# Kernel tuning notes

Measured on AMD Instinct MI355X. Metric: run time of the kernel, lower is better.

The kernel has to match this reference:

```python
import jax, jax.numpy as jnp
import numpy as np

B, S, H = 4, 2048, 1024
NH = 16
HD = H // NH  # 64
EPS = 1e-12


def setup_inputs() -> dict:
    key = jax.random.key(0)
    ks = jax.random.split(key, 10)
    sc = 1.0 / np.sqrt(H)
    return {
        "hidden_states": jax.random.normal(ks[0], (B, S, H), jnp.float32),
        "attention_mask": jnp.ones((B, S), jnp.float32),
        "Wq": jax.random.normal(ks[1], (H, H), jnp.float32) * sc,
        "bq": jnp.zeros((H,), jnp.float32),
        "Wk": jax.random.normal(ks[2], (H, H), jnp.float32) * sc,
        "bk": jnp.zeros((H,), jnp.float32),
        "Wv": jax.random.normal(ks[3], (H, H), jnp.float32) * sc,
        "bv": jnp.zeros((H,), jnp.float32),
        "Wd": jax.random.normal(ks[4], (H, H), jnp.float32) * sc,
        "bd": jnp.zeros((H,), jnp.float32),
        "ln_g": jnp.ones((H,), jnp.float32),
        "ln_b": jnp.zeros((H,), jnp.float32),
    }


def reference(hidden_states, attention_mask, Wq, bq, Wk, bk, Wv, bv, Wd, bd, ln_g, ln_b):
    def heads(x):  # [B,S,H] -> [B,NH,S,HD]
        return x.reshape(B, S, NH, HD).transpose(0, 2, 1, 3)

    q = heads(hidden_states @ Wq.T + bq)
    k = heads(hidden_states @ Wk.T + bk)
    v = heads(hidden_states @ Wv.T + bv)

    scores = jnp.einsum('bhqd,bhkd->bhqk', q, k) / np.sqrt(HD).astype(np.float32)
    # 2D mask -> [B,1,1,S]; (1-m)*-10000 additive bias
    bias = (1.0 - attention_mask)[:, None, None, :] * -10000.0
    probs = jax.nn.softmax(scores + bias, axis=-1)  # dropout p=0 -> identity

    ctx = jnp.einsum('bhqk,bhkd->bhqd', probs, v)
    ctx = ctx.transpose(0, 2, 1, 3).reshape(B, S, H)

    out = ctx @ Wd.T + bd
    x = out + hidden_states
    mu = jnp.mean(x, axis=-1, keepdims=True)
    var = jnp.mean(jnp.square(x - mu), axis=-1, keepdims=True)
    return (x - mu) * jax.lax.rsqrt(var + EPS) * ln_g + ln_b
```

## Files before the change

### kernel.cpp

```cpp
#include <hip/hip_runtime.h>
#include <stdint.h>

#define B_ 4
#define S_ 2048
#define H_ 1024
#define NH_ 16
#define HD_ 64

typedef __bf16 bf16x8 __attribute__((ext_vector_type(8)));
typedef unsigned short u16x8 __attribute__((ext_vector_type(8)));
typedef float f32x4 __attribute__((ext_vector_type(4)));
typedef float f32x16 __attribute__((ext_vector_type(16)));

__device__ __forceinline__ unsigned short f2bf(float x) {
  union { float f; unsigned u; } c; c.f = x;
  unsigned r = (c.u + 0x7FFFu + ((c.u >> 16) & 1u)) >> 16;
  return (unsigned short)r;
}

__device__ __forceinline__ void gload16(const unsigned short* g, unsigned short* lds) {
  __builtin_amdgcn_global_load_lds((const __attribute__((address_space(1))) void*)g,
                                   (__attribute__((address_space(3))) void*)lds, 16, 0, 0);
}

__global__ __launch_bounds__(256) void cvt_kernel(const float* __restrict__ src,
                                                  unsigned short* __restrict__ dst, int n) {
  int i = (blockIdx.x * blockDim.x + threadIdx.x) * 4;
  if (i < n) {
    float4 v = *reinterpret_cast<const float4*>(src + i);
    ushort4 o;
    o.x = f2bf(v.x); o.y = f2bf(v.y); o.z = f2bf(v.z); o.w = f2bf(v.w);
    *reinterpret_cast<ushort4*>(dst + i) = o;
  }
}

template <bool BF16OUT>
__global__ __launch_bounds__(256) void gemm_bt(const unsigned short* __restrict__ A,
                                               const unsigned short* __restrict__ Bm,
                                               const float* __restrict__ bias,
                                               void* __restrict__ Cout,
                                               int M, int N, int K) {
  __shared__ unsigned short As[128 * 32];
  __shared__ unsigned short Bs[128 * 32];
  const int t = threadIdx.x;
  const int lane = t & 63;
  const int wv = t >> 6;
  const int wm = wv >> 1, wn = wv & 1;
  const int m0 = blockIdx.x * 128, n0 = blockIdx.y * 128;
  const int l15 = lane & 15, g8 = (lane >> 4) * 8;

  f32x4 acc[4][4];
#pragma unroll
  for (int i = 0; i < 4; ++i)
#pragma unroll
    for (int j = 0; j < 4; ++j) { f32x4 z = {0.f, 0.f, 0.f, 0.f}; acc[i][j] = z; }

  const int rowA = t >> 2;
  const int colA = (t & 3) * 8;
  const unsigned short* gA0 = A + (long)(m0 + rowA) * K + colA;
  const unsigned short* gA1 = A + (long)(m0 + 64 + rowA) * K + colA;
  const unsigned short* gB0 = Bm + (long)(n0 + rowA) * K + colA;
  const unsigned short* gB1 = Bm + (long)(n0 + 64 + rowA) * K + colA;
  unsigned short* ldsA0 = &As[wv * 512];
  unsigned short* ldsA1 = &As[2048 + wv * 512];
  unsigned short* ldsB0 = &Bs[wv * 512];
  unsigned short* ldsB1 = &Bs[2048 + wv * 512];

  for (int k0 = 0; k0 < K; k0 += 32) {
    __syncthreads();
    gload16(gA0 + k0, ldsA0);
    gload16(gA1 + k0, ldsA1);
    gload16(gB0 + k0, ldsB0);
    gload16(gB1 + k0, ldsB1);
    __syncthreads();

    bf16x8 af[4], bfr[4];
#pragma unroll
    for (int i = 0; i < 4; ++i)
      af[i] = *reinterpret_cast<const bf16x8*>(&As[(wm * 64 + i * 16 + l15) * 32 + g8]);
#pragma unroll
    for (int j = 0; j < 4; ++j)
      bfr[j] = *reinterpret_cast<const bf16x8*>(&Bs[(wn * 64 + j * 16 + l15) * 32 + g8]);
#pragma unroll
    for (int i = 0; i < 4; ++i)
#pragma unroll
      for (int j = 0; j < 4; ++j)
        acc[i][j] = __builtin_amdgcn_mfma_f32_16x16x32_bf16(af[i], bfr[j], acc[i][j], 0, 0, 0);
  }

  const int r0 = (lane >> 4) * 4;
#pragma unroll
  for (int i = 0; i < 4; ++i)
#pragma unroll
    for (int j = 0; j < 4; ++j) {
      int col = n0 + wn * 64 + j * 16 + l15;
      float bv = bias[col];
#pragma unroll
      for (int r = 0; r < 4; ++r) {
        int row = m0 + wm * 64 + i * 16 + r0 + r;
        float v = acc[i][j][r] + bv;
        if (BF16OUT)
          ((unsigned short*)Cout)[(long)row * N + col] = f2bf(v);
        else
          ((float*)Cout)[(long)row * N + col] = v;
      }
    }
}

__global__ __launch_bounds__(256) void attn_kernel(const unsigned short* __restrict__ Q,
                                                   const unsigned short* __restrict__ Kg,
                                                   const unsigned short* __restrict__ Vg,
                                                   const float* __restrict__ mask,
                                                   unsigned short* __restrict__ ctx) {
  __shared__ __align__(16) unsigned short Kt[64 * 72];
  __shared__ __align__(16) unsigned short VtT[64 * 72];
  __shared__ __align__(16) float biasL[64];
  __shared__ __align__(16) float alBuf[4][32];
  __shared__ int mflag;

  const int t = threadIdx.x, lane = t & 63;
  const int wv = t >> 6;
  const int h = blockIdx.y, b = blockIdx.z;
  const int q0w = blockIdx.x * 128 + wv * 32;
  const int l31 = lane & 31, h2 = lane >> 5;
  const long headoff = (long)h * HD_;
  const float L2E = 1.44269504088896f;
  const float SC = 0.125f * L2E;

  bf16x8 qf[4];
  {
    const unsigned short* Qrow = Q + ((long)(b * S_ + q0w + l31)) * H_ + headoff;
#pragma unroll
    for (int c = 0; c < 4; ++c) {
      bf16x8 raw = *reinterpret_cast<const bf16x8*>(Qrow + 16 * c + 8 * h2);
#pragma unroll
      for (int j = 0; j < 8; ++j) qf[c][j] = (__bf16)((float)raw[j] * SC);
    }
  }

  f32x16 o[2];
#pragma unroll
  for (int dt = 0; dt < 2; ++dt)
#pragma unroll
    for (int r = 0; r < 16; ++r) o[dt][r] = 0.f;
  float mrow = -1.0e30f, lsum = 0.f;

  const unsigned short* KtA = &Kt[l31 * 72 + 8 * h2];
  const int rowd0 = l31, rowd1 = 32 + l31;
  const int grp0 = (rowd0 >> 3) & 7, grp1 = (rowd1 >> 3) & 7;

  for (int kv0 = 0; kv0 < S_; kv0 += 64) {
    __syncthreads();
#pragma unroll
    for (int it = 0; it < 2; ++it) {
      int job = t + it * 256;
      int kv = job >> 3, cg = (job & 7) * 8;
      u16x8 kvv = *reinterpret_cast<const u16x8*>(
          Kg + ((long)(b * S_ + kv0 + kv)) * H_ + headoff + cg);
      *reinterpret_cast<u16x8*>(&Kt[kv * 72 + cg]) = kvv;
    }
    {
      int p2 = t >> 3, dc = t & 7;
      int kv = p2 * 2;
      const unsigned short* vp0 = Vg + ((long)(b * S_ + kv0 + kv)) * H_ + headoff + dc * 8;
      u16x8 v0 = *reinterpret_cast<const u16x8*>(vp0);
      u16x8 v1 = *reinterpret_cast<const u16x8*>(vp0 + H_);
      int pos = (kv & 7) | (((kv >> 3) ^ dc) << 3);
#pragma unroll
      for (int j = 0; j < 8; ++j) {
        ushort2 pr; pr.x = v0[j]; pr.y = v1[j];
        *reinterpret_cast<ushort2*>(&VtT[(dc * 8 + j) * 72 + pos]) = pr;
      }
    }
    if (t < 64) {
      float mv = mask[b * S_ + kv0 + t];
      bool nz = (mv != 1.0f);
      biasL[t] = (1.f - mv) * (-10000.f * L2E);
      unsigned long long bal = __ballot(nz);
      if (t == 0) mflag = (bal != 0ull);
    }
    __syncthreads();

#pragma unroll
    for (int kvt = 0; kvt < 2; ++kvt) {
      f32x16 sv;
#pragma unroll
      for (int r = 0; r < 16; ++r) sv[r] = 0.f;
#pragma unroll
      for (int c = 0; c < 4; ++c) {
        bf16x8 af = *reinterpret_cast<const bf16x8*>(KtA + (kvt * 32) * 72 + 16 * c);
        sv = __builtin_amdgcn_mfma_f32_32x32x16_bf16(af, qf[c], sv, 0, 0, 0);
      }
      if (mflag) {
#pragma unroll
        for (int m = 0; m < 4; ++m) {
          f32x4 bb = *reinterpret_cast<const f32x4*>(&biasL[kvt * 32 + 8 * m + 4 * h2]);
#pragma unroll
          for (int i = 0; i < 4; ++i) sv[4 * m + i] += bb[i];
        }
      }
      float tm = sv[0];
#pragma unroll
      for (int r = 1; r < 16; ++r) tm = fmaxf(tm, sv[r]);
      tm = fmaxf(tm, __shfl_xor(tm, 32));
      if (!__all(tm <= mrow + 8.0f)) {
        float mn = fmaxf(mrow, tm);
        float al = exp2f(mrow - mn);
        mrow = mn;
        lsum *= al;
        if (lane < 32) alBuf[wv][lane] = al;
        __builtin_amdgcn_wave_barrier();
#pragma unroll
        for (int m = 0; m < 4; ++m) {
          f32x4 av = *reinterpret_cast<const f32x4*>(&alBuf[wv][8 * m + 4 * h2]);
#pragma unroll
          for (int i = 0; i < 4; ++i) {
            o[0][4 * m + i] *= av[i];
            o[1][4 * m + i] *= av[i];
          }
        }
      }
      float ts = 0.f;
#pragma unroll
      for (int r = 0; r < 16; ++r) {
        float p = exp2f(sv[r] - mrow);
        sv[r] = p;
        ts += p;
      }
      ts += __shfl_xor(ts, 32);
      lsum += ts;

#pragma unroll
      for (int c2 = 0; c2 < 2; ++c2) {
        int kc = 2 * kvt + c2;
        unsigned p0, p1, p2, p3;
        {
          union { __bf16 e[2]; unsigned w; } u;
          u.e[0] = (__bf16)sv[8 * c2 + 0]; u.e[1] = (__bf16)sv[8 * c2 + 1]; p0 = u.w;
          u.e[0] = (__bf16)sv[8 * c2 + 2]; u.e[1] = (__bf16)sv[8 * c2 + 3]; p1 = u.w;
          u.e[0] = (__bf16)sv[8 * c2 + 4]; u.e[1] = (__bf16)sv[8 * c2 + 5]; p2 = u.w;
          u.e[0] = (__bf16)sv[8 * c2 + 6]; u.e[1] = (__bf16)sv[8 * c2 + 7]; p3 = u.w;
        }
        asm("v_permlane32_swap_b32 %0, %1" : "+v"(p0), "+v"(p2));
        asm("v_permlane32_swap_b32 %0, %1" : "+v"(p1), "+v"(p3));
        union { unsigned w[4]; bf16x8 v; } fa;
        fa.w[0] = p0; fa.w[1] = p1; fa.w[2] = p2; fa.w[3] = p3;

        bf16x8 vb0 = *reinterpret_cast<const bf16x8*>(
            &VtT[rowd0 * 72 + 8 * ((2 * kc + h2) ^ grp0)]);
        bf16x8 vb1 = *reinterpret_cast<const bf16x8*>(
            &VtT[rowd1 * 72 + 8 * ((2 * kc + h2) ^ grp1)]);
        o[0] = __builtin_amdgcn_mfma_f32_32x32x16_bf16(fa.v, vb0, o[0], 0, 0, 0);
        o[1] = __builtin_amdgcn_mfma_f32_32x32x16_bf16(fa.v, vb1, o[1], 0, 0, 0);
      }
    }
  }

  if (lane < 32) alBuf[wv][lane] = 1.0f / lsum;
  __builtin_amdgcn_wave_barrier();
  unsigned short* ctxbase = ctx + ((long)(b * S_ + q0w + 4 * h2)) * H_ + headoff + l31;
#pragma unroll
  for (int m = 0; m < 4; ++m) {
    f32x4 iv = *reinterpret_cast<const f32x4*>(&alBuf[wv][8 * m + 4 * h2]);
#pragma unroll
    for (int i = 0; i < 4; ++i) {
#pragma unroll
      for (int dt = 0; dt < 2; ++dt)
        ctxbase[(long)(8 * m + i) * H_ + dt * 32] = f2bf(o[dt][4 * m + i] * iv[i]);
    }
  }
}

__global__ __launch_bounds__(256) void ln_kernel(const float* __restrict__ proj,
                                                 const float* __restrict__ hs,
                                                 const float* __restrict__ gam,
                                                 const float* __restrict__ bet,
                                                 float* __restrict__ out) {
  const int row = blockIdx.x;
  const int t = threadIdx.x;
  const long base = (long)row * H_ + t * 4;
  float4 a = *reinterpret_cast<const float4*>(proj + base);
  float4 hv = *reinterpret_cast<const float4*>(hs + base);
  float x0 = a.x + hv.x, x1 = a.y + hv.y, x2 = a.z + hv.z, x3 = a.w + hv.w;
  float s1 = x0 + x1 + x2 + x3;
  float s2 = x0 * x0 + x1 * x1 + x2 * x2 + x3 * x3;
#pragma unroll
  for (int off = 1; off < 64; off <<= 1) {
    s1 += __shfl_xor(s1, off);
    s2 += __shfl_xor(s2, off);
  }
  __shared__ float a1[4], a2[4];
  if ((t & 63) == 0) { a1[t >> 6] = s1; a2[t >> 6] = s2; }
  __syncthreads();
  float ts1 = a1[0] + a1[1] + a1[2] + a1[3];
  float ts2 = a2[0] + a2[1] + a2[2] + a2[3];
  float mu = ts1 * (1.0f / H_);
  float var = ts2 * (1.0f / H_) - mu * mu;
  float inv = rsqrtf(var + 1e-12f);
  float4 gv = *reinterpret_cast<const float4*>(gam + t * 4);
  float4 bb = *reinterpret_cast<const float4*>(bet + t * 4);
  float4 ov;
  ov.x = (x0 - mu) * inv * gv.x + bb.x;
  ov.y = (x1 - mu) * inv * gv.y + bb.y;
  ov.z = (x2 - mu) * inv * gv.z + bb.z;
  ov.w = (x3 - mu) * inv * gv.w + bb.w;
  *reinterpret_cast<float4*>(out + base) = ov;
}

extern "C" void kernel_launch(void* const* d_in, const int* in_sizes, int n_in,
                              void* d_out, int out_size, void* d_ws, size_t ws_size,
                              hipStream_t stream) {
  const float* hs   = (const float*)d_in[0];
  const float* mask = (const float*)d_in[1];
  const float* Wq   = (const float*)d_in[2];
  const float* bq   = (const float*)d_in[3];
  const float* Wk   = (const float*)d_in[4];
  const float* bk   = (const float*)d_in[5];
  const float* Wv   = (const float*)d_in[6];
  const float* bv   = (const float*)d_in[7];
  const float* Wd   = (const float*)d_in[8];
  const float* bd   = (const float*)d_in[9];
  const float* lng  = (const float*)d_in[10];
  const float* lnb  = (const float*)d_in[11];
  float* out = (float*)d_out;

  char* ws = (char*)d_ws;
  const size_t SZ_X = (size_t)B_ * S_ * H_ * 2;
  const size_t SZ_W = (size_t)H_ * H_ * 2;
  unsigned short* Xb  = (unsigned short*)(ws);
  unsigned short* Wqb = (unsigned short*)(ws + SZ_X);
  unsigned short* Wkb = (unsigned short*)(ws + SZ_X + SZ_W);
  unsigned short* Wvb = (unsigned short*)(ws + SZ_X + 2 * SZ_W);
  unsigned short* Wdb = (unsigned short*)(ws + SZ_X + 3 * SZ_W);
  unsigned short* Qb  = (unsigned short*)(ws + SZ_X + 4 * SZ_W);
  unsigned short* Kb  = (unsigned short*)(ws + 2 * SZ_X + 4 * SZ_W);
  unsigned short* Vb  = (unsigned short*)(ws + 3 * SZ_X + 4 * SZ_W);
  unsigned short* Cxb = (unsigned short*)(ws + 4 * SZ_X + 4 * SZ_W);
  float* Proj         = (float*)(ws + 5 * SZ_X + 4 * SZ_W);

  const int NX = B_ * S_ * H_;
  const int NW = H_ * H_;

  cvt_kernel<<<NX / 1024, 256, 0, stream>>>(hs, Xb, NX);
  cvt_kernel<<<NW / 1024, 256, 0, stream>>>(Wq, Wqb, NW);
  cvt_kernel<<<NW / 1024, 256, 0, stream>>>(Wk, Wkb, NW);
  cvt_kernel<<<NW / 1024, 256, 0, stream>>>(Wv, Wvb, NW);
  cvt_kernel<<<NW / 1024, 256, 0, stream>>>(Wd, Wdb, NW);

  dim3 gg(B_ * S_ / 128, H_ / 128);
  gemm_bt<true><<<gg, 256, 0, stream>>>(Xb, Wqb, bq, Qb, B_ * S_, H_, H_);
  gemm_bt<true><<<gg, 256, 0, stream>>>(Xb, Wkb, bk, Kb, B_ * S_, H_, H_);
  gemm_bt<true><<<gg, 256, 0, stream>>>(Xb, Wvb, bv, Vb, B_ * S_, H_, H_);

  dim3 ga(S_ / 128, NH_, B_);
  attn_kernel<<<ga, 256, 0, stream>>>(Qb, Kb, Vb, mask, Cxb);

  gemm_bt<false><<<gg, 256, 0, stream>>>(Cxb, Wdb, bd, Proj, B_ * S_, H_, H_);

  ln_kernel<<<B_ * S_, 256, 0, stream>>>(Proj, hs, lng, lnb, out);
}
```

Before: 330.7 us.

## Double-buffer K/V tiles in attention with register prefetch and MFMA priority

Converts the attention kernel's K/V/mask staging to a two-buffer scheme. The next tile's global loads go into registers before the current tile's compute and are written to the alternate LDS buffer afterward, with one barrier per iteration instead of two. It also raises wave priority around the MFMA blocks and rewrites the max and sum reductions as trees to shorten dependency chains. The cost is doubled LDS use and extra live registers for the prefetch, which may reduce occupancy.

Measured after the change: 311.9 us. 5.7% less time.

```diff
diff --git a/kernel.cpp b/kernel.cpp
--- a/kernel.cpp
+++ b/kernel.cpp
@@ -112,11 +112,11 @@
                                                    const unsigned short* __restrict__ Vg,
                                                    const float* __restrict__ mask,
                                                    unsigned short* __restrict__ ctx) {
-  __shared__ __align__(16) unsigned short Kt[64 * 72];
-  __shared__ __align__(16) unsigned short VtT[64 * 72];
-  __shared__ __align__(16) float biasL[64];
+  __shared__ __align__(16) unsigned short Kt[2][64 * 72];
+  __shared__ __align__(16) unsigned short VtT[2][64 * 72];
+  __shared__ __align__(16) float biasL[2][64];
   __shared__ __align__(16) float alBuf[4][32];
-  __shared__ int mflag;
+  __shared__ int mflag[2];
 
   const int t = threadIdx.x, lane = t & 63;
   const int wv = t >> 6;
@@ -145,63 +145,77 @@
     for (int r = 0; r < 16; ++r) o[dt][r] = 0.f;
   float mrow = -1.0e30f, lsum = 0.f;
 
-  const unsigned short* KtA = &Kt[l31 * 72 + 8 * h2];
   const int rowd0 = l31, rowd1 = 32 + l31;
   const int grp0 = (rowd0 >> 3) & 7, grp1 = (rowd1 >> 3) & 7;
 
-  for (int kv0 = 0; kv0 < S_; kv0 += 64) {
-    __syncthreads();
-#pragma unroll
-    for (int it = 0; it < 2; ++it) {
-      int job = t + it * 256;
-      int kv = job >> 3, cg = (job & 7) * 8;
-      u16x8 kvv = *reinterpret_cast<const u16x8*>(
-          Kg + ((long)(b * S_ + kv0 + kv)) * H_ + headoff + cg);
-      *reinterpret_cast<u16x8*>(&Kt[kv * 72 + cg]) = kvv;
-    }
-    {
-      int p2 = t >> 3, dc = t & 7;
-      int kv = p2 * 2;
-      const unsigned short* vp0 = Vg + ((long)(b * S_ + kv0 + kv)) * H_ + headoff + dc * 8;
-      u16x8 v0 = *reinterpret_cast<const u16x8*>(vp0);
-      u16x8 v1 = *reinterpret_cast<const u16x8*>(vp0 + H_);
-      int pos = (kv & 7) | (((kv >> 3) ^ dc) << 3);
-#pragma unroll
-      for (int j = 0; j < 8; ++j) {
-        ushort2 pr; pr.x = v0[j]; pr.y = v1[j];
-        *reinterpret_cast<ushort2*>(&VtT[(dc * 8 + j) * 72 + pos]) = pr;
-      }
+  const int krow = t >> 3, kcg = (t & 7) * 8;
+  const int vrow = (t >> 3) * 2, dc = t & 7;
+  const long gbase = (long)(b * S_) * H_ + headoff;
+  u16x8 kr0, kr1, vr0, vr1;
+  float mv = 1.0f;
+
+  auto LOADT = [&](int kv0) {
+    kr0 = *reinterpret_cast<const u16x8*>(Kg + gbase + (long)(kv0 + krow) * H_ + kcg);
+    kr1 = *reinterpret_cast<const u16x8*>(Kg + gbase + (long)(kv0 + krow + 32) * H_ + kcg);
+    vr0 = *reinterpret_cast<const u16x8*>(Vg + gbase + (long)(kv0 + vrow) * H_ + dc * 8);
+    vr1 = *reinterpret_cast<const u16x8*>(Vg + gbase + (long)(kv0 + vrow + 1) * H_ + dc * 8);
+    if (t < 64) mv = mask[b * S_ + kv0 + t];
+  };
+  auto WRITET = [&](int buf) {
+    *reinterpret_cast<u16x8*>(&Kt[buf][krow * 72 + kcg]) = kr0;
+    *reinterpret_cast<u16x8*>(&Kt[buf][(krow + 32) * 72 + kcg]) = kr1;
+    const int pos = (vrow & 7) | (((vrow >> 3) ^ dc) << 3);
+#pragma unroll
+    for (int j = 0; j < 8; ++j) {
+      ushort2 pr; pr.x = vr0[j]; pr.y = vr1[j];
+      *reinterpret_cast<ushort2*>(&VtT[buf][(dc * 8 + j) * 72 + pos]) = pr;
     }
     if (t < 64) {
-      float mv = mask[b * S_ + kv0 + t];
-      bool nz = (mv != 1.0f);
-      biasL[t] = (1.f - mv) * (-10000.f * L2E);
-      unsigned long long bal = __ballot(nz);
-      if (t == 0) mflag = (bal != 0ull);
-    }
-    __syncthreads();
+      biasL[buf][t] = (1.f - mv) * (-10000.f * L2E);
+      unsigned long long bal = __ballot(mv != 1.0f);
+      if (t == 0) mflag[buf] = (bal != 0ull);
+    }
+  };
+
+  const int NT = S_ / 64;
+  LOADT(0);
+  WRITET(0);
+  __syncthreads();
+
+  for (int it = 0; it < NT; ++it) {
+    const int cur = it & 1;
+    const bool more = (it + 1 < NT);
+    if (more) LOADT((it + 1) * 64);
+
+    const unsigned short* KtA = &Kt[cur][l31 * 72 + 8 * h2];
+    const int mf = mflag[cur];
 
 #pragma unroll
     for (int kvt = 0; kvt < 2; ++kvt) {
       f32x16 sv;
 #pragma unroll
       for (int r = 0; r < 16; ++r) sv[r] = 0.f;
+      __builtin_amdgcn_s_setprio(1);
 #pragma unroll
       for (int c = 0; c < 4; ++c) {
         bf16x8 af = *reinterpret_cast<const bf16x8*>(KtA + (kvt * 32) * 72 + 16 * c);
         sv = __builtin_amdgcn_mfma_f32_32x32x16_bf16(af, qf[c], sv, 0, 0, 0);
       }
-      if (mflag) {
+      __builtin_amdgcn_s_setprio(0);
+      if (mf) {
 #pragma unroll
         for (int m = 0; m < 4; ++m) {
-          f32x4 bb = *reinterpret_cast<const f32x4*>(&biasL[kvt * 32 + 8 * m + 4 * h2]);
+          f32x4 bb = *reinterpret_cast<const f32x4*>(&biasL[cur][kvt * 32 + 8 * m + 4 * h2]);
 #pragma unroll
           for (int i = 0; i < 4; ++i) sv[4 * m + i] += bb[i];
         }
       }
-      float tm = sv[0];
-#pragma unroll
-      for (int r = 1; r < 16; ++r) tm = fmaxf(tm, sv[r]);
+      float a0 = fmaxf(sv[0], sv[1]), a1 = fmaxf(sv[2], sv[3]);
+      float a2 = fmaxf(sv[4], sv[5]), a3 = fmaxf(sv[6], sv[7]);
+      float a4 = fmaxf(sv[8], sv[9]), a5 = fmaxf(sv[10], sv[11]);
+      float a6 = fmaxf(sv[12], sv[13]), a7 = fmaxf(sv[14], sv[15]);
+      float b0 = fmaxf(a0, a1), b1 = fmaxf(a2, a3), b2 = fmaxf(a4, a5), b3 = fmaxf(a6, a7);
+      float tm = fmaxf(fmaxf(b0, b1), fmaxf(b2, b3));
       tm = fmaxf(tm, __shfl_xor(tm, 32));
       if (!__all(tm <= mrow + 8.0f)) {
         float mn = fmaxf(mrow, tm);
@@ -220,15 +234,16 @@
           }
         }
       }
-      float ts = 0.f;
-#pragma unroll
-      for (int r = 0; r < 16; ++r) {
-        float p = exp2f(sv[r] - mrow);
-        sv[r] = p;
-        ts += p;
-      }
-      ts += __shfl_xor(ts, 32);
-      lsum += ts;
+#pragma unroll
+      for (int r = 0; r < 16; ++r) sv[r] = exp2f(sv[r] - mrow);
+      {
+        float s0 = sv[0] + sv[1], s1 = sv[2] + sv[3], s2 = sv[4] + sv[5], s3 = sv[6] + sv[7];
+        float s4 = sv[8] + sv[9], s5 = sv[10] + sv[11], s6 = sv[12] + sv[13], s7 = sv[14] + sv[15];
+        float u0 = s0 + s1, u1 = s2 + s3, u2 = s4 + s5, u3 = s6 + s7;
+        float ts = (u0 + u1) + (u2 + u3);
+        ts += __shfl_xor(ts, 32);
+        lsum += ts;
+      }
 
 #pragma unroll
       for (int c2 = 0; c2 < 2; ++c2) {
@@ -247,12 +262,19 @@
         fa.w[0] = p0; fa.w[1] = p1; fa.w[2] = p2; fa.w[3] = p3;
 
         bf16x8 vb0 = *reinterpret_cast<const bf16x8*>(
-            &VtT[rowd0 * 72 + 8 * ((2 * kc + h2) ^ grp0)]);
+            &VtT[cur][rowd0 * 72 + 8 * ((2 * kc + h2) ^ grp0)]);
         bf16x8 vb1 = *reinterpret_cast<const bf16x8*>(
-            &VtT[rowd1 * 72 + 8 * ((2 * kc + h2) ^ grp1)]);
+            &VtT[cur][rowd1 * 72 + 8 * ((2 * kc + h2) ^ grp1)]);
+        __builtin_amdgcn_s_setprio(1);
         o[0] = __builtin_amdgcn_mfma_f32_32x32x16_bf16(fa.v, vb0, o[0], 0, 0, 0);
         o[1] = __builtin_amdgcn_mfma_f32_32x32x16_bf16(fa.v, vb1, o[1], 0, 0, 0);
-      }
+        __builtin_amdgcn_s_setprio(0);
+      }
+    }
+
+    if (more) {
+      WRITET(cur ^ 1);
+      __syncthreads();
     }
   }
 
```
